# Performance work log

Hardware: AMD Instinct MI355X
Metric: run time of the kernel (lower is better)

## Reference

```python
import jax, jax.numpy as jnp
import numpy as np

N_NODES = 100000


def setup_inputs() -> dict:
    key = jax.random.key(0)
    ks = jax.random.split(key, 6)
    F_IN, F_CH, F_OUT = 64, 64, 64
    E = 1200000
    x = jax.random.normal(ks[0], (N_NODES, F_IN), dtype=jnp.float32)
    edge_index = jax.random.randint(ks[1], (2, E), 0, N_NODES, dtype=jnp.int64)
    # MLP params (PyTorch Linear default init scale ~ 1/sqrt(fan_in))
    s1 = 1.0 / np.sqrt(2 * F_IN)
    s2 = 1.0 / np.sqrt(F_CH)
    W1 = jax.random.uniform(ks[2], (2 * F_IN, F_CH), jnp.float32, -s1, s1)
    b1 = jax.random.uniform(ks[3], (F_CH,), jnp.float32, -s1, s1)
    W2 = jax.random.uniform(ks[4], (F_CH, F_OUT), jnp.float32, -s2, s2)
    b2 = jax.random.uniform(ks[5], (F_OUT,), jnp.float32, -s2, s2)
    return {"x": x, "edge_index": edge_index, "W1": W1, "b1": b1, "W2": W2, "b2": b2}


def reference(x, edge_index, W1, b1, W2, b2):
    # PyG EdgeConv with aggr='add': out_i = sum_j MLP(concat[x_i, x_j - x_i])
    src = edge_index[0]  # j (source / neighbor)
    dst = edge_index[1]  # i (target, aggregation index)
    x_i = x[dst]                     # [E, F]
    x_j = x[src]                     # [E, F]
    msg = jnp.concatenate([x_i, x_j - x_i], axis=-1)      # [E, 2F]
    h = jax.nn.relu(msg @ W1 + b1) @ W2 + b2               # [E, F_out]
    agg = jax.ops.segment_sum(h, dst, num_segments=N_NODES)  # [N, F_out]
    return jnp.tanh(agg)
```

## Files before the change

kernel.cpp:

```cpp
#include <hip/hip_runtime.h>
#include <math.h>


#define FDIM 64
#define BN 64
#define BSH 6
#define CAPB 1024
#define MAXB 2048
#define EPB 4096
#define PRE_SMEM 16384

typedef unsigned int u32;
typedef unsigned short u16;
typedef _Float16 hf;
typedef _Float16 h2 __attribute__((ext_vector_type(2)));

__device__ __forceinline__ float bf_lo(u32 u) {
    union { u32 i; float f; } c; c.i = u << 16; return c.f;
}
__device__ __forceinline__ float bf_hi(u32 u) {
    union { u32 i; float f; } c; c.i = u & 0xffff0000u; return c.f;
}
__device__ __forceinline__ u32 f2bf_rne(float f) {
    union { float f; u32 u; } c; c.f = f;
    u32 u = c.u;
    u += 0x7fffu + ((u >> 16) & 1u);
    return u >> 16;
}
__device__ __forceinline__ u32 f2h(float f) {
    union { u16 s; hf h; } c; c.h = (hf)f; return (u32)c.s;
}
__device__ __forceinline__ float h_lo(u32 u) {
    union { u16 s; hf h; } c; c.s = (u16)(u & 0xffffu); return (float)c.h;
}
__device__ __forceinline__ float h_hi(u32 u) {
    union { u16 s; hf h; } c; c.s = (u16)(u >> 16); return (float)c.h;
}
__device__ __forceinline__ h2 u2h2(u32 u) {
    union { u32 u; h2 h; } c; c.u = u; return c.h;
}

__global__ __launch_bounds__(256) void prep_k(
    const float* __restrict__ x, const float* __restrict__ W1,
    u16* __restrict__ Bmh, const int* __restrict__ ei,
    u32* __restrict__ slotB, int* __restrict__ gcnt,
    int N, int E, int NB, int nPre, int nBin)
{
    __shared__ __align__(16) char smem[PRE_SMEM];
    const int idx = blockIdx.x;
    const int tid = threadIdx.x;

    if ((idx % 6) == 5) {
        const int bb = idx / 6;
        if (bb >= nBin) return;
        int* histL = (int*)smem;
        int* gbase = histL + MAXB;
        const int e0 = bb * EPB;

        for (int j = tid; j < NB; j += 256) histL[j] = 0;
        __syncthreads();

        #pragma unroll 8
        for (int i = 0; i < EPB / 256; ++i) {
            int e = e0 + i * 256 + tid;
            if (e < E) {
                int d = ei[E + e];
                atomicAdd(&histL[d >> BSH], 1);
            }
        }
        __syncthreads();

        for (int j = tid; j < NB; j += 256) {
            int h = histL[j];
            gbase[j] = (h > 0) ? atomicAdd(&gcnt[j], h) : 0;
            histL[j] = 0;
        }
        __syncthreads();

        #pragma unroll 8
        for (int i = 0; i < EPB / 256; ++i) {
            int e = e0 + i * 256 + tid;
            if (e < E) {
                int s = ei[e];
                int d = ei[E + e];
                int b = d >> BSH;
                int pos = gbase[b] + atomicAdd(&histL[b], 1);
                if (pos < CAPB)
                    slotB[(size_t)b * CAPB + pos] =
                        ((u32)(d & (BN - 1)) << 20) | (u32)s;
            }
        }
        return;
    }

    const int pb = idx - idx / 6;
    if (pb >= nPre) return;
    u32 (*Wch)[64] = (u32(*)[64])smem;
    u32* xs = (u32*)(smem + 8192);

    const int node0 = pb * 64;

    for (int i = tid; i < 2048; i += 256) {
        int kk = i >> 6, c = i & 63;
        float a0 = W1[(64 + 2 * kk) * 64 + c];
        float a1 = W1[(64 + 2 * kk + 1) * 64 + c];
        ((u32*)smem)[i] = f2h(a0) | (f2h(a1) << 16);
    }
    {
        const float4* X4 = (const float4*)x;
        #pragma unroll
        for (int it = 0; it < 4; ++it) {
            int i = it * 256 + tid;
            int n = i >> 4, k4 = i & 15;
            int gn = node0 + n;
            float4 v = make_float4(0.f, 0.f, 0.f, 0.f);
            if (gn < N) v = X4[(size_t)gn * 16 + k4];
            int r0 = 2 * k4, r1 = r0 + 1;
            int g = n >> 2, lo = n & 3;
            xs[r0 * 64 + (((g ^ (r0 & 15)) << 2) | lo)] = f2h(v.x) | (f2h(v.y) << 16);
            xs[r1 * 64 + (((g ^ (r1 & 15)) << 2) | lo)] = f2h(v.z) | (f2h(v.w) << 16);
        }
    }
    __syncthreads();

    const int ng = tid & 15, cg = tid >> 4;
    const int n0 = ng * 4, c0 = cg * 4;

    float acc[4][4];
    #pragma unroll
    for (int ni = 0; ni < 4; ++ni)
        #pragma unroll
        for (int ci = 0; ci < 4; ++ci) acc[ni][ci] = 0.f;

    #pragma unroll 4
    for (int kk = 0; kk < 32; ++kk) {
        uint4 xq = *(const uint4*)&xs[kk * 64 + ((ng ^ (kk & 15)) << 2)];
        uint4 w = *(const uint4*)&Wch[kk][c0];
        h2 wv[4] = {u2h2(w.x), u2h2(w.y), u2h2(w.z), u2h2(w.w)};
        u32 xq4[4] = {xq.x, xq.y, xq.z, xq.w};
        #pragma unroll
        for (int ni = 0; ni < 4; ++ni) {
            h2 xh = u2h2(xq4[ni]);
            #pragma unroll
            for (int ci = 0; ci < 4; ++ci)
                acc[ni][ci] = __builtin_amdgcn_fdot2(xh, wv[ci], acc[ni][ci], false);
        }
    }

    #pragma unroll
    for (int ni = 0; ni < 4; ++ni) {
        int n = node0 + n0 + ni;
        if (n >= N) break;
        uint2 pk;
        pk.x = f2bf_rne(acc[ni][0]) | (f2bf_rne(acc[ni][1]) << 16);
        pk.y = f2bf_rne(acc[ni][2]) | (f2bf_rne(acc[ni][3]) << 16);
        *(uint2*)&Bmh[(size_t)n * 64 + c0] = pk;
    }
}

__device__ __forceinline__ float4 relu4add(float4 acc, float4 a, float4 b) {
    acc.x += fmaxf(a.x + b.x, 0.f);
    acc.y += fmaxf(a.y + b.y, 0.f);
    acc.z += fmaxf(a.z + b.z, 0.f);
    acc.w += fmaxf(a.w + b.w, 0.f);
    return acc;
}
__device__ __forceinline__ float4 relu4add_m(float4 acc, float4 a, float4 b, bool m) {
    acc.x += m ? fmaxf(a.x + b.x, 0.f) : 0.f;
    acc.y += m ? fmaxf(a.y + b.y, 0.f) : 0.f;
    acc.z += m ? fmaxf(a.z + b.z, 0.f) : 0.f;
    acc.w += m ? fmaxf(a.w + b.w, 0.f) : 0.f;
    return acc;
}
__device__ __forceinline__ float4 bf4(uint2 u) {
    return make_float4(bf_lo(u.x), bf_hi(u.x), bf_lo(u.y), bf_hi(u.y));
}

__global__ __launch_bounds__(256) void fused_agg(
    const float* __restrict__ x, const float* __restrict__ W1,
    const float* __restrict__ b1, const u16* __restrict__ Bmh,
    const u32* __restrict__ slotB, const int* __restrict__ gcnt,
    const float* __restrict__ W2, const float* __restrict__ b2,
    float* __restrict__ out, int N)
{
    __shared__ __align__(16) char uni[16384];
    __shared__ __align__(16) u32 W2h[64][34];
    __shared__ int histL[BN];
    __shared__ int rowO[BN + 1];
    __shared__ int ofs[BN];
    __shared__ float b2s[64];
    __shared__ float b1s[64];

    u32 (*Wdh)[64] = (u32(*)[64])uni;
    u32* xs = (u32*)(uni + 8192);
    u32* csrS = (u32*)uni;
    u32* eStage = (u32*)(uni + 4096);
    uint2* aggTb = (uint2*)(uni + 4096);

    const int tid = threadIdx.x;
    const int b = blockIdx.x;
    const int node0 = b * BN;
    const int cntB = min(gcnt[b], CAPB);

    for (int i = tid; i < 2048; i += 256) {
        int kk = i >> 6, c = i & 63;
        int k0 = 2 * kk, k1 = k0 + 1;
        float a0 = W1[k0 * 64 + c] - W1[(64 + k0) * 64 + c];
        float a1 = W1[k1 * 64 + c] - W1[(64 + k1) * 64 + c];
        ((u32*)uni)[i] = f2h(a0) | (f2h(a1) << 16);
    }
    {
        const float4* X4 = (const float4*)x;
        #pragma unroll
        for (int it = 0; it < 4; ++it) {
            int i = it * 256 + tid;
            int n = i >> 4, k4 = i & 15;
            int gn = node0 + n;
            float4 v = make_float4(0.f, 0.f, 0.f, 0.f);
            if (gn < N) v = X4[(size_t)gn * 16 + k4];
            int r0 = 2 * k4, r1 = r0 + 1;
            int g = n >> 2, lo = n & 3;
            xs[r0 * 64 + (((g ^ (r0 & 15)) << 2) | lo)] = f2h(v.x) | (f2h(v.y) << 16);
            xs[r1 * 64 + (((g ^ (r1 & 15)) << 2) | lo)] = f2h(v.z) | (f2h(v.w) << 16);
        }
    }
    for (int i = tid; i < 2048; i += 256) {
        int k = i >> 5, c2 = i & 31;
        W2h[k][c2] = f2h(W2[k * 64 + 2 * c2]) | (f2h(W2[k * 64 + 2 * c2 + 1]) << 16);
    }
    if (tid < 64) { b2s[tid] = b2[tid]; b1s[tid] = b1[tid]; }
    if (tid < BN) histL[tid] = 0;
    __syncthreads();

    const int q = tid & 15, ng = tid >> 4;
    const int q4 = q * 4;
    float af[4][4];
    #pragma unroll
    for (int h = 0; h < 4; ++h)
        #pragma unroll
        for (int ci = 0; ci < 4; ++ci) af[h][ci] = b1s[q4 + ci];

    #pragma unroll 4
    for (int kk = 0; kk < 32; ++kk) {
        uint4 wq = *(const uint4*)&Wdh[kk][q4];
        h2 wv[4] = {u2h2(wq.x), u2h2(wq.y), u2h2(wq.z), u2h2(wq.w)};
        #pragma unroll
        for (int h = 0; h < 4; ++h) {
            int n = ng + h * 16;
            int g = n >> 2, lo = n & 3;
            u32 xv = xs[kk * 64 + (((g ^ (kk & 15)) << 2) | lo)];
            h2 xh = u2h2(xv);
            #pragma unroll
            for (int ci = 0; ci < 4; ++ci)
                af[h][ci] = __builtin_amdgcn_fdot2(xh, wv[ci], af[h][ci], false);
        }
    }
    __syncthreads();

    for (int i = tid; i < cntB; i += 256) {
        u32 e = slotB[(size_t)b * CAPB + i];
        eStage[i] = e;
        atomicAdd(&histL[e >> 20], 1);
    }
    __syncthreads();

    if (tid < 32) {
        int l = tid;
        int h0 = histL[2 * l], h1 = histL[2 * l + 1];
        int s = h0 + h1, inc = s;
        #pragma unroll
        for (int off = 1; off < 32; off <<= 1) {
            int t = __shfl_up(inc, off);
            if (l >= off) inc += t;
        }
        int base = inc - s;
        rowO[2 * l] = base; rowO[2 * l + 1] = base + h0;
        ofs[2 * l] = base;  ofs[2 * l + 1] = base + h0;
        if (l == 31) rowO[BN] = inc;
    }
    __syncthreads();

    for (int i = tid; i < cntB; i += 256) {
        u32 e = eStage[i];
        int pos = atomicAdd(&ofs[e >> 20], 1);
        csrS[pos] = e & 0xFFFFFu;
    }
    __syncthreads();

    {
        const uint2* __restrict__ B2 = (const uint2*)Bmh;
        #pragma unroll
        for (int h = 0; h < 4; ++h) {
            int nl = ng + h * 16;
            int gn = node0 + nl;
            int start = rowO[nl];
            int d = (gn < N) ? (rowO[nl + 1] - start) : 0;
            float4 a = make_float4(af[h][0], af[h][1], af[h][2], af[h][3]);
            float4 acc = make_float4(0.f, 0.f, 0.f, 0.f);

            int j = 0;
            for (; j + 8 <= d; j += 8) {
                int ss[8];
                uint2 bb[8];
                #pragma unroll
                for (int t = 0; t < 8; ++t) ss[t] = csrS[start + j + t];
                #pragma unroll
                for (int t = 0; t < 8; ++t) bb[t] = B2[(size_t)ss[t] * 16 + q];
                #pragma unroll
                for (int t = 0; t < 8; ++t) acc = relu4add(acc, a, bf4(bb[t]));
            }
            if (j < d) {
                int ss[8];
                uint2 bb[8];
                #pragma unroll
                for (int t = 0; t < 8; ++t) ss[t] = csrS[start + min(j + t, d - 1)];
                #pragma unroll
                for (int t = 0; t < 8; ++t) bb[t] = B2[(size_t)ss[t] * 16 + q];
                acc = relu4add(acc, a, bf4(bb[0]));
                #pragma unroll
                for (int t = 1; t < 8; ++t)
                    acc = relu4add_m(acc, a, bf4(bb[t]), j + t < d);
            }
            uint2 pk;
            pk.x = f2h(acc.x) | (f2h(acc.y) << 16);
            pk.y = f2h(acc.z) | (f2h(acc.w) << 16);
            aggTb[nl * 17 + q] = pk;
        }
    }
    __syncthreads();

    {
        const int cg = tid & 15, g = tid >> 4;
        const int c0 = cg * 4;
        const int nb0 = g * 4;
        float o[4][4];
        #pragma unroll
        for (int ni = 0; ni < 4; ++ni) {
            float dg = (float)(rowO[nb0 + ni + 1] - rowO[nb0 + ni]);
            #pragma unroll
            for (int ci = 0; ci < 4; ++ci) o[ni][ci] = dg * b2s[c0 + ci];
        }
        #pragma unroll 2
        for (int kc = 0; kc < 16; ++kc) {
            uint2 u0 = aggTb[(nb0 + 0) * 17 + kc];
            uint2 u1 = aggTb[(nb0 + 1) * 17 + kc];
            uint2 u2 = aggTb[(nb0 + 2) * 17 + kc];
            uint2 u3 = aggTb[(nb0 + 3) * 17 + kc];
            #pragma unroll
            for (int kk = 0; kk < 4; ++kk) {
                uint2 w2p = *(const uint2*)&W2h[kc * 4 + kk][cg * 2];
                float wv[4] = {h_lo(w2p.x), h_hi(w2p.x), h_lo(w2p.y), h_hi(w2p.y)};
                float a0 = (kk < 2) ? ((kk == 0) ? h_lo(u0.x) : h_hi(u0.x))
                                    : ((kk == 2) ? h_lo(u0.y) : h_hi(u0.y));
                float a1 = (kk < 2) ? ((kk == 0) ? h_lo(u1.x) : h_hi(u1.x))
                                    : ((kk == 2) ? h_lo(u1.y) : h_hi(u1.y));
                float a2 = (kk < 2) ? ((kk == 0) ? h_lo(u2.x) : h_hi(u2.x))
                                    : ((kk == 2) ? h_lo(u2.y) : h_hi(u2.y));
                float a3 = (kk < 2) ? ((kk == 0) ? h_lo(u3.x) : h_hi(u3.x))
                                    : ((kk == 2) ? h_lo(u3.y) : h_hi(u3.y));
                #pragma unroll
                for (int ci = 0; ci < 4; ++ci) {
                    o[0][ci] += a0 * wv[ci];
                    o[1][ci] += a1 * wv[ci];
                    o[2][ci] += a2 * wv[ci];
                    o[3][ci] += a3 * wv[ci];
                }
            }
        }
        #pragma unroll
        for (int ni = 0; ni < 4; ++ni) {
            int gn = node0 + nb0 + ni;
            if (gn < N) {
                float4 r = make_float4(tanhf(o[ni][0]), tanhf(o[ni][1]),
                                       tanhf(o[ni][2]), tanhf(o[ni][3]));
                ((float4*)out)[(size_t)gn * 16 + cg] = r;
            }
        }
    }
}

extern "C" void kernel_launch(void* const* d_in, const int* in_sizes, int n_in,
                              void* d_out, int out_size, void* d_ws, size_t ws_size,
                              hipStream_t stream)
{
    const float* x  = (const float*)d_in[0];
    const int*   ei = (const int*)d_in[1];
    const float* W1 = (const float*)d_in[2];
    const float* b1 = (const float*)d_in[3];
    const float* W2 = (const float*)d_in[4];
    const float* b2 = (const float*)d_in[5];
    float* out = (float*)d_out;

    const int N = in_sizes[0] / FDIM;
    const int E = in_sizes[1] / 2;
    const int NB = (N + BN - 1) / BN;

    u16*   Bmh   = (u16*)d_ws;
    u32*   slotB = (u32*)(Bmh + (size_t)N * FDIM);
    int*   gcnt  = (int*)(slotB + (size_t)NB * CAPB);

    hipMemsetAsync(gcnt, 0, (size_t)NB * sizeof(int), stream);

    const int nPre = (N + 63) / 64;
    const int nBin = (E + EPB - 1) / EPB;
    int T = (nPre * 6 + 4) / 5;
    while (T - T / 6 < nPre) ++T;
    if (T < 6 * nBin) T = 6 * nBin;

    prep_k<<<T, 256, 0, stream>>>(x, W1, Bmh, ei, slotB, gcnt,
                                  N, E, NB, nPre, nBin);
    fused_agg<<<NB, 256, 0, stream>>>(x, W1, b1, Bmh, slotB, gcnt, W2, b2, out, N);
}
```

Before: 185.6 us.

## Use packed fp16 math for edge aggregation and W2 projection

Stores the per-node B projection in fp16 instead of bf16 and performs the per-edge add+relu with packed half2 ops. Accumulation is done through fdot2 with selector vectors. The W2 projection is rewritten to use fdot2 on k-paired packed weights, and the node-to-thread mapping is changed so each thread reads a contiguous uint4 of x. The goal is to cut ALU work in the gather-heavy inner loop and the epilogue, at the cost of fp16 range and rounding in the per-edge sums.

```diff
diff --git a/kernel.cpp b/kernel.cpp
--- a/kernel.cpp
+++ b/kernel.cpp
@@ -15,26 +15,8 @@
 typedef _Float16 hf;
 typedef _Float16 h2 __attribute__((ext_vector_type(2)));
 
-__device__ __forceinline__ float bf_lo(u32 u) {
-    union { u32 i; float f; } c; c.i = u << 16; return c.f;
-}
-__device__ __forceinline__ float bf_hi(u32 u) {
-    union { u32 i; float f; } c; c.i = u & 0xffff0000u; return c.f;
-}
-__device__ __forceinline__ u32 f2bf_rne(float f) {
-    union { float f; u32 u; } c; c.f = f;
-    u32 u = c.u;
-    u += 0x7fffu + ((u >> 16) & 1u);
-    return u >> 16;
-}
 __device__ __forceinline__ u32 f2h(float f) {
     union { u16 s; hf h; } c; c.h = (hf)f; return (u32)c.s;
-}
-__device__ __forceinline__ float h_lo(u32 u) {
-    union { u16 s; hf h; } c; c.s = (u16)(u & 0xffffu); return (float)c.h;
-}
-__device__ __forceinline__ float h_hi(u32 u) {
-    union { u16 s; hf h; } c; c.s = (u16)(u >> 16); return (float)c.h;
 }
 __device__ __forceinline__ h2 u2h2(u32 u) {
     union { u32 u; h2 h; } c; c.u = u; return c.h;
@@ -152,28 +134,10 @@
         int n = node0 + n0 + ni;
         if (n >= N) break;
         uint2 pk;
-        pk.x = f2bf_rne(acc[ni][0]) | (f2bf_rne(acc[ni][1]) << 16);
-        pk.y = f2bf_rne(acc[ni][2]) | (f2bf_rne(acc[ni][3]) << 16);
+        pk.x = f2h(acc[ni][0]) | (f2h(acc[ni][1]) << 16);
+        pk.y = f2h(acc[ni][2]) | (f2h(acc[ni][3]) << 16);
         *(uint2*)&Bmh[(size_t)n * 64 + c0] = pk;
     }
-}
-
-__device__ __forceinline__ float4 relu4add(float4 acc, float4 a, float4 b) {
-    acc.x += fmaxf(a.x + b.x, 0.f);
-    acc.y += fmaxf(a.y + b.y, 0.f);
-    acc.z += fmaxf(a.z + b.z, 0.f);
-    acc.w += fmaxf(a.w + b.w, 0.f);
-    return acc;
-}
-__device__ __forceinline__ float4 relu4add_m(float4 acc, float4 a, float4 b, bool m) {
-    acc.x += m ? fmaxf(a.x + b.x, 0.f) : 0.f;
-    acc.y += m ? fmaxf(a.y + b.y, 0.f) : 0.f;
-    acc.z += m ? fmaxf(a.z + b.z, 0.f) : 0.f;
-    acc.w += m ? fmaxf(a.w + b.w, 0.f) : 0.f;
-    return acc;
-}
-__device__ __forceinline__ float4 bf4(uint2 u) {
-    return make_float4(bf_lo(u.x), bf_hi(u.x), bf_lo(u.y), bf_hi(u.y));
 }
 
 __global__ __launch_bounds__(256) void fused_agg(
@@ -184,7 +148,7 @@
     float* __restrict__ out, int N)
 {
     __shared__ __align__(16) char uni[16384];
-    __shared__ __align__(16) u32 W2h[64][34];
+    __shared__ __align__(16) u32 W2kp[2048];
     __shared__ int histL[BN];
     __shared__ int rowO[BN + 1];
     __shared__ int ofs[BN];
@@ -225,8 +189,8 @@
         }
     }
     for (int i = tid; i < 2048; i += 256) {
-        int k = i >> 5, c2 = i & 31;
-        W2h[k][c2] = f2h(W2[k * 64 + 2 * c2]) | (f2h(W2[k * 64 + 2 * c2 + 1]) << 16);
+        int kk = i >> 6, c = i & 63;
+        W2kp[i] = f2h(W2[(2 * kk) * 64 + c]) | (f2h(W2[(2 * kk + 1) * 64 + c]) << 16);
     }
     if (tid < 64) { b2s[tid] = b2[tid]; b1s[tid] = b1[tid]; }
     if (tid < BN) histL[tid] = 0;
@@ -242,18 +206,23 @@
 
     #pragma unroll 4
     for (int kk = 0; kk < 32; ++kk) {
+        uint4 xq = *(const uint4*)&xs[kk * 64 + ((ng ^ (kk & 15)) << 2)];
         uint4 wq = *(const uint4*)&Wdh[kk][q4];
         h2 wv[4] = {u2h2(wq.x), u2h2(wq.y), u2h2(wq.z), u2h2(wq.w)};
+        u32 xq4[4] = {xq.x, xq.y, xq.z, xq.w};
         #pragma unroll
         for (int h = 0; h < 4; ++h) {
-            int n = ng + h * 16;
-            int g = n >> 2, lo = n & 3;
-            u32 xv = xs[kk * 64 + (((g ^ (kk & 15)) << 2) | lo)];
-            h2 xh = u2h2(xv);
+            h2 xh = u2h2(xq4[h]);
             #pragma unroll
             for (int ci = 0; ci < 4; ++ci)
                 af[h][ci] = __builtin_amdgcn_fdot2(xh, wv[ci], af[h][ci], false);
         }
+    }
+    u32 pa[4][2];
+    #pragma unroll
+    for (int h = 0; h < 4; ++h) {
+        pa[h][0] = f2h(af[h][0]) | (f2h(af[h][1]) << 16);
+        pa[h][1] = f2h(af[h][2]) | (f2h(af[h][3]) << 16);
     }
     __syncthreads();
 
@@ -289,14 +258,17 @@
 
     {
         const uint2* __restrict__ B2 = (const uint2*)Bmh;
+        const h2 SEL10 = {(_Float16)1.f, (_Float16)0.f};
+        const h2 SEL01 = {(_Float16)0.f, (_Float16)1.f};
+        const h2 HZ = {(_Float16)0.f, (_Float16)0.f};
         #pragma unroll
         for (int h = 0; h < 4; ++h) {
-            int nl = ng + h * 16;
+            int nl = ng * 4 + h;
             int gn = node0 + nl;
             int start = rowO[nl];
             int d = (gn < N) ? (rowO[nl + 1] - start) : 0;
-            float4 a = make_float4(af[h][0], af[h][1], af[h][2], af[h][3]);
-            float4 acc = make_float4(0.f, 0.f, 0.f, 0.f);
+            h2 A0 = u2h2(pa[h][0]), A1 = u2h2(pa[h][1]);
+            float ac0 = 0.f, ac1 = 0.f, ac2 = 0.f, ac3 = 0.f;
 
             int j = 0;
             for (; j + 8 <= d; j += 8) {
@@ -307,7 +279,16 @@
                 #pragma unroll
                 for (int t = 0; t < 8; ++t) bb[t] = B2[(size_t)ss[t] * 16 + q];
                 #pragma unroll
-                for (int t = 0; t < 8; ++t) acc = relu4add(acc, a, bf4(bb[t]));
+                for (int t = 0; t < 8; ++t) {
+                    h2 t0 = A0 + u2h2(bb[t].x);
+                    h2 t1 = A1 + u2h2(bb[t].y);
+                    t0 = __builtin_elementwise_max(t0, HZ);
+                    t1 = __builtin_elementwise_max(t1, HZ);
+                    ac0 = __builtin_amdgcn_fdot2(t0, SEL10, ac0, false);
+                    ac1 = __builtin_amdgcn_fdot2(t0, SEL01, ac1, false);
+                    ac2 = __builtin_amdgcn_fdot2(t1, SEL10, ac2, false);
+                    ac3 = __builtin_amdgcn_fdot2(t1, SEL01, ac3, false);
+                }
             }
             if (j < d) {
                 int ss[8];
@@ -316,14 +297,22 @@
                 for (int t = 0; t < 8; ++t) ss[t] = csrS[start + min(j + t, d - 1)];
                 #pragma unroll
                 for (int t = 0; t < 8; ++t) bb[t] = B2[(size_t)ss[t] * 16 + q];
-                acc = relu4add(acc, a, bf4(bb[0]));
-                #pragma unroll
-                for (int t = 1; t < 8; ++t)
-                    acc = relu4add_m(acc, a, bf4(bb[t]), j + t < d);
+                #pragma unroll
+                for (int t = 0; t < 8; ++t) {
+                    if (j + t >= d) { bb[t].x = 0xFC00FC00u; bb[t].y = 0xFC00FC00u; }
+                    h2 t0 = A0 + u2h2(bb[t].x);
+                    h2 t1 = A1 + u2h2(bb[t].y);
+                    t0 = __builtin_elementwise_max(t0, HZ);
+                    t1 = __builtin_elementwise_max(t1, HZ);
+                    ac0 = __builtin_amdgcn_fdot2(t0, SEL10, ac0, false);
+                    ac1 = __builtin_amdgcn_fdot2(t0, SEL01, ac1, false);
+                    ac2 = __builtin_amdgcn_fdot2(t1, SEL10, ac2, false);
+                    ac3 = __builtin_amdgcn_fdot2(t1, SEL01, ac3, false);
+                }
             }
             uint2 pk;
-            pk.x = f2h(acc.x) | (f2h(acc.y) << 16);
-            pk.y = f2h(acc.z) | (f2h(acc.w) << 16);
+            pk.x = f2h(ac0) | (f2h(ac1) << 16);
+            pk.y = f2h(ac2) | (f2h(ac3) << 16);
             aggTb[nl * 17 + q] = pk;
         }
     }
@@ -340,31 +329,30 @@
             #pragma unroll
             for (int ci = 0; ci < 4; ++ci) o[ni][ci] = dg * b2s[c0 + ci];
         }
-        #pragma unroll 2
+        #pragma unroll 4
         for (int kc = 0; kc < 16; ++kc) {
             uint2 u0 = aggTb[(nb0 + 0) * 17 + kc];
             uint2 u1 = aggTb[(nb0 + 1) * 17 + kc];
             uint2 u2 = aggTb[(nb0 + 2) * 17 + kc];
             uint2 u3 = aggTb[(nb0 + 3) * 17 + kc];
+            uint4 wA = *(const uint4*)&W2kp[(2 * kc) * 64 + c0];
+            uint4 wB = *(const uint4*)&W2kp[(2 * kc + 1) * 64 + c0];
+            h2 wa[4] = {u2h2(wA.x), u2h2(wA.y), u2h2(wA.z), u2h2(wA.w)};
+            h2 wb[4] = {u2h2(wB.x), u2h2(wB.y), u2h2(wB.z), u2h2(wB.w)};
+            h2 a0x = u2h2(u0.x), a0y = u2h2(u0.y);
+            h2 a1x = u2h2(u1.x), a1y = u2h2(u1.y);
+            h2 a2x = u2h2(u2.x), a2y = u2h2(u2.y);
+            h2 a3x = u2h2(u3.x), a3y = u2h2(u3.y);
             #pragma unroll
-            for (int kk = 0; kk < 4; ++kk) {
-                uint2 w2p = *(const uint2*)&W2h[kc * 4 + kk][cg * 2];
-                float wv[4] = {h_lo(w2p.x), h_hi(w2p.x), h_lo(w2p.y), h_hi(w2p.y)};
-                float a0 = (kk < 2) ? ((kk == 0) ? h_lo(u0.x) : h_hi(u0.x))
-                                    : ((kk == 2) ? h_lo(u0.y) : h_hi(u0.y));
-                float a1 = (kk < 2) ? ((kk == 0) ? h_lo(u1.x) : h_hi(u1.x))
-                                    : ((kk == 2) ? h_lo(u1.y) : h_hi(u1.y));
-                float a2 = (kk < 2) ? ((kk == 0) ? h_lo(u2.x) : h_hi(u2.x))
-                                    : ((kk == 2) ? h_lo(u2.y) : h_hi(u2.y));
-                float a3 = (kk < 2) ? ((kk == 0) ? h_lo(u3.x) : h_hi(u3.x))
-                                    : ((kk == 2) ? h_lo(u3.y) : h_hi(u3.y));
-                #pragma unroll
-                for (int ci = 0; ci < 4; ++ci) {
-                    o[0][ci] += a0 * wv[ci];
-                    o[1][ci] += a1 * wv[ci];
-                    o[2][ci] += a2 * wv[ci];
-                    o[3][ci] += a3 * wv[ci];
-                }
+            for (int ci = 0; ci < 4; ++ci) {
+                o[0][ci] = __builtin_amdgcn_fdot2(a0x, wa[ci], o[0][ci], false);
+                o[0][ci] = __builtin_amdgcn_fdot2(a0y, wb[ci], o[0][ci], false);
+                o[1][ci] = __builtin_amdgcn_fdot2(a1x, wa[ci], o[1][ci], false);
+                o[1][ci] = __builtin_amdgcn_fdot2(a1y, wb[ci], o[1][ci], false);
+                o[2][ci] = __builtin_amdgcn_fdot2(a2x, wa[ci], o[2][ci], false);
+                o[2][ci] = __builtin_amdgcn_fdot2(a2y, wb[ci], o[2][ci], false);
+                o[3][ci] = __builtin_amdgcn_fdot2(a3x, wa[ci], o[3][ci], false);
+                o[3][ci] = __builtin_amdgcn_fdot2(a3y, wb[ci], o[3][ci], false);
             }
         }
         #pragma unroll
```

Result: faster. 171.0 us (-7.8%).
